# Optimization experiments

Measured on AMD Instinct MI355X. Metric: run time of the kernel, lower is better.

## Reference

```python
import jax, jax.numpy as jnp
import numpy as np
from math import factorial, sqrt

# ---- e3nn-style real Wigner-3j (Clebsch-Gordan) construction ----
L1, L2, LOUT, LMID = 3, 3, 3, 4

def _cg_coef(j1, m1, j2, m2, j3, m3):
    if m1 + m2 != m3:
        return 0.0
    f = factorial
    vmin = max(0, j2 - j3 - m1, j1 - j3 + m2)
    vmax = min(j1 + j2 - j3, j1 - m1, j2 + m2)
    pref = sqrt((2 * j3 + 1) * f(j3 + j1 - j2) * f(j3 - j1 + j2) * f(j1 + j2 - j3) / f(j1 + j2 + j3 + 1))
    pref *= sqrt(f(j3 + m3) * f(j3 - m3) * f(j1 + m1) * f(j1 - m1) * f(j2 + m2) * f(j2 - m2))
    s = 0.0
    for v in range(vmin, vmax + 1):
        s += (-1) ** v / (f(v) * f(j1 + j2 - j3 - v) * f(j1 - m1 - v) * f(j2 + m2 - v)
                          * f(j3 - j2 + m1 + v) * f(j3 - j1 - m2 + v))
    return pref * s

def _su2_cg(l1, l2, l3):
    C = np.zeros((2 * l1 + 1, 2 * l2 + 1, 2 * l3 + 1))
    for m1 in range(-l1, l1 + 1):
        for m2 in range(-l2, l2 + 1):
            m3 = m1 + m2
            if -l3 <= m3 <= l3:
                C[l1 + m1, l2 + m2, l3 + m3] = _cg_coef(l1, m1, l2, m2, l3, m3)
    return C

def _q(l):  # real->complex SH change of basis (e3nn convention)
    q = np.zeros((2 * l + 1, 2 * l + 1), dtype=np.complex128)
    for m in range(-l, 0):
        q[l + m, l + abs(m)] = 1 / np.sqrt(2)
        q[l + m, l - abs(m)] = -1j / np.sqrt(2)
    q[l, l] = 1.0
    for m in range(1, l + 1):
        q[l + m, l + abs(m)] = (-1) ** m / np.sqrt(2)
        q[l + m, l - abs(m)] = 1j * (-1) ** m / np.sqrt(2)
    return (-1j) ** l * q

def _w3j(l1, l2, l3):
    C = _su2_cg(l1, l2, l3).astype(np.complex128)
    C = np.einsum('ij,kl,mn,ikn->jlm', _q(l1), _q(l2), np.conj(_q(l3).T), C)
    C = np.real(C)
    return (C / np.linalg.norm(C)).astype(np.float32)

def _instructions(lmax1, lmax2, lmax_out):
    ins = [(a, b, c)
           for a in range(lmax1 + 1) for b in range(lmax2 + 1) for c in range(lmax_out + 1)
           if abs(a - b) <= c <= a + b and (a + b + c) % 2 == 0]
    cnt = {}
    for _, _, c in ins:
        cnt[c] = cnt.get(c, 0) + 1
    # normalization='component', path_normalization='element' with all mul=1
    pw = np.array([sqrt((2 * c + 1) / cnt[c]) for _, _, c in ins], dtype=np.float32)
    return ins, pw

INS1, PW1 = _instructions(L1, L2, LMID)      # 27 paths
INS21, PW21 = _instructions(L1, LMID, LOUT)  # 27 paths
INS22, PW22 = _instructions(L2, LMID, LOUT)  # 27 paths
W3J = {k: jnp.asarray(_w3j(*k)) for k in set(INS1) | set(INS21) | set(INS22)}

def _tp(x, y, w, ins, pw, lmax_out):
    # FullyConnectedTensorProduct with multiplicity-1 SH irreps.
    # x: [E, (l1+1)^2], y: [E, (l2+1)^2] -> [E, (lmax_out+1)^2]
    out = jnp.zeros((x.shape[0], (lmax_out + 1) ** 2), dtype=x.dtype)
    for i, (a, b, c) in enumerate(ins):
        xa = x[:, a * a:(a + 1) ** 2]
        yb = y[:, b * b:(b + 1) ** 2]
        z = jnp.einsum('ijk,ei,ej->ek', W3J[(a, b, c)], xa, yb)
        out = out.at[:, c * c:(c + 1) ** 2].add((pw[i] * w[i]) * z)
    return out

E, C = 200000, 16
B = (LOUT + 1) ** 2  # 16

def setup_inputs() -> dict:
    k = jax.random.split(jax.random.key(0), 5)
    return {
        'x': jax.random.normal(k[0], (E, B, C), jnp.float32),
        'y': jax.random.normal(k[1], (E, B, C), jnp.float32),
        'w1': jax.random.normal(k[2], (len(INS1),), jnp.float32),
        'w21': jax.random.normal(k[3], (len(INS21),), jnp.float32),
        'w22': jax.random.normal(k[4], (len(INS22),), jnp.float32),
    }

def reference(x, y, w1, w21, w22):
    xm = x.mean(2)  # [E, 16]
    ym = y.mean(2)  # [E, 16]
    mid = _tp(xm, ym, w1, INS1, PW1, LMID)  # [E, 25]
    out = (x + y
           + _tp(xm, mid, w21, INS21, PW21, LOUT)[..., None]
           + _tp(ym, mid, w22, INS22, PW22, LOUT)[..., None])
    return out
```

## Files before the change

### kernel.cpp

```cpp
#include <hip/hip_runtime.h>


struct W3JT { double v[9][9][9]; };

constexpr double dfact(int n) { double r = 1.0; for (int i = 2; i <= n; ++i) r *= (double)i; return r; }

constexpr double csqrt(double x) {
  if (x <= 0.0) return 0.0;
  double g = x > 1.0 ? x : 1.0;
  for (int i = 0; i < 80; ++i) g = 0.5 * (g + x / g);
  return g;
}

constexpr double cg_coef(int j1, int m1, int j2, int m2, int j3, int m3) {
  if (m1 + m2 != m3) return 0.0;
  int vmin = 0;
  if (j2 - j3 - m1 > vmin) vmin = j2 - j3 - m1;
  if (j1 - j3 + m2 > vmin) vmin = j1 - j3 + m2;
  int vmax = j1 + j2 - j3;
  if (j1 - m1 < vmax) vmax = j1 - m1;
  if (j2 + m2 < vmax) vmax = j2 + m2;
  double pref = csqrt((2.0 * j3 + 1.0) * dfact(j3 + j1 - j2) * dfact(j3 - j1 + j2) * dfact(j1 + j2 - j3) / dfact(j1 + j2 + j3 + 1));
  pref *= csqrt(dfact(j3 + m3) * dfact(j3 - m3) * dfact(j1 + m1) * dfact(j1 - m1) * dfact(j2 + m2) * dfact(j2 - m2));
  double s = 0.0;
  for (int v = vmin; v <= vmax; ++v) {
    double t = 1.0 / (dfact(v) * dfact(j1 + j2 - j3 - v) * dfact(j1 - m1 - v) * dfact(j2 + m2 - v) * dfact(j3 - j2 + m1 + v) * dfact(j3 - j1 - m2 + v));
    s += (v & 1) ? -t : t;
  }
  return pref * s;
}

struct QCol { int n; int row[2]; double re[2]; double im[2]; };

constexpr QCol qcol(int l, int col) {
  QCol q{};
  const int lm = l & 3;
  const double pr = (lm == 0) ? 1.0 : (lm == 2) ? -1.0 : 0.0;
  const double pi = (lm == 1) ? -1.0 : (lm == 3) ? 1.0 : 0.0;
  const int mu = col - l;
  const int am = mu < 0 ? -mu : mu;
  const double is2 = 0.70710678118654752440;
  if (mu == 0) {
    q.n = 1; q.row[0] = l;
    q.re[0] = pr; q.im[0] = pi;
  } else {
    const double s = (am & 1) ? -1.0 : 1.0;
    double a0 = 0.0, b0 = 0.0, a1 = 0.0, b1 = 0.0;
    if (mu > 0) { a0 = is2; b0 = 0.0;  a1 = s * is2; b1 = 0.0; }
    else        { a0 = 0.0; b0 = -is2; a1 = 0.0;     b1 = s * is2; }
    q.n = 2;
    q.row[0] = l - am; q.row[1] = l + am;
    q.re[0] = a0 * pr - b0 * pi; q.im[0] = a0 * pi + b0 * pr;
    q.re[1] = a1 * pr - b1 * pi; q.im[1] = a1 * pi + b1 * pr;
  }
  return q;
}

constexpr W3JT make_w3j(int l1, int l2, int l3) {
  W3JT R{};
  double C[9][9][9]{};
  for (int m1 = -l1; m1 <= l1; ++m1)
    for (int m2 = -l2; m2 <= l2; ++m2) {
      int m3 = m1 + m2;
      if (m3 >= -l3 && m3 <= l3)
        C[l1 + m1][l2 + m2][l3 + m3] = cg_coef(l1, m1, l2, m2, l3, m3);
    }
  double nrm = 0.0;
  for (int j = 0; j < 2 * l1 + 1; ++j) {
    QCol q1 = qcol(l1, j);
    for (int l = 0; l < 2 * l2 + 1; ++l) {
      QCol q2 = qcol(l2, l);
      for (int m = 0; m < 2 * l3 + 1; ++m) {
        QCol q3 = qcol(l3, m);
        double re = 0.0;
        for (int a = 0; a < q1.n; ++a)
          for (int b = 0; b < q2.n; ++b)
            for (int c = 0; c < q3.n; ++c) {
              double cv = C[q1.row[a]][q2.row[b]][q3.row[c]];
              if (cv == 0.0) continue;
              double ar = q1.re[a], ai = q1.im[a];
              double br = q2.re[b], bi = q2.im[b];
              double cr = q3.re[c], ci = -q3.im[c];
              double abr = ar * br - ai * bi;
              double abi = ar * bi + ai * br;
              double prr = abr * cr - abi * ci;
              re += prr * cv;
            }
        R.v[j][l][m] = re;
        nrm += re * re;
      }
    }
  }
  double n = csqrt(nrm);
  if (n > 0.0)
    for (int j = 0; j < 2 * l1 + 1; ++j)
      for (int l = 0; l < 2 * l2 + 1; ++l)
        for (int m = 0; m < 2 * l3 + 1; ++m)
          R.v[j][l][m] /= n;
  return R;
}

constexpr int CNT1[5] = {4, 6, 7, 6, 4};
constexpr int CNT2[4] = {4, 7, 8, 8};

#define NZCHK(V) ((V) > 1e-12 || (V) < -1e-12)

#define TP_MID(IDX, A, B, C) do { \
  constexpr W3JT T = make_w3j(A, B, C); \
  constexpr double PW = csqrt((2.0 * (C) + 1.0) / (double)CNT1[(C)]); \
  const float wi = w1p[IDX]; \
  float u[2 * (A) + 1]; \
  _Pragma("unroll") for (int i = 0; i < 2 * (A) + 1; ++i) u[i] = wi * xm[(A) * (A) + i]; \
  _Pragma("unroll") for (int i = 0; i < 2 * (A) + 1; ++i) { \
    _Pragma("unroll") for (int j = 0; j < 2 * (B) + 1; ++j) { \
      const float p_ = u[i] * ym[(B) * (B) + j]; \
      _Pragma("unroll") for (int k = 0; k < 2 * (C) + 1; ++k) { \
        if (NZCHK(T.v[i][j][k])) \
          mid[(C) * (C) + k] = __builtin_fmaf((float)(T.v[i][j][k] * PW), p_, mid[(C) * (C) + k]); \
      } \
    } \
  } \
} while (0)

#define TP_OUT(IDX, A, B, C) do { \
  constexpr W3JT T = make_w3j(A, B, C); \
  constexpr double PW = csqrt((2.0 * (C) + 1.0) / (double)CNT2[(C)]); \
  const float wa = w21p[IDX]; \
  const float wb = w22p[IDX]; \
  float u[2 * (A) + 1]; \
  _Pragma("unroll") for (int i = 0; i < 2 * (A) + 1; ++i) \
    u[i] = wa * xm[(A) * (A) + i] + wb * ym[(A) * (A) + i]; \
  _Pragma("unroll") for (int i = 0; i < 2 * (A) + 1; ++i) { \
    _Pragma("unroll") for (int j = 0; j < 2 * (B) + 1; ++j) { \
      const float p_ = u[i] * mid[(B) * (B) + j]; \
      _Pragma("unroll") for (int k = 0; k < 2 * (C) + 1; ++k) { \
        if (NZCHK(T.v[i][j][k])) \
          tv[(C) * (C) + k] = __builtin_fmaf((float)(T.v[i][j][k] * PW), p_, tv[(C) * (C) + k]); \
      } \
    } \
  } \
} while (0)

__global__ __launch_bounds__(256) void cg2_v6(
    const float4* __restrict__ x4, const float4* __restrict__ y4,
    const float* __restrict__ w1p, const float* __restrict__ w21p,
    const float* __restrict__ w22p, float4* __restrict__ o4, int E)
{
  __shared__ float lmx[64 * 32];
  __shared__ float ltv[64 * 16];

  const int eL = threadIdx.x >> 2;
  const int g  = threadIdx.x & 3;
  const int e  = blockIdx.x * 64 + eL;
  const bool ok = (e < E);
  const int base = e * 64 + g;

  float4 s[16];
  float px[16], py[16];
  if (ok) {
#pragma unroll
    for (int k = 0; k < 16; ++k) {
      const float4 xv = x4[base + 4 * k];
      const float4 yv = y4[base + 4 * k];
      s[k].x = xv.x + yv.x; s[k].y = xv.y + yv.y;
      s[k].z = xv.z + yv.z; s[k].w = xv.w + yv.w;
      px[k] = (xv.x + xv.y) + (xv.z + xv.w);
      py[k] = (yv.x + yv.y) + (yv.z + yv.w);
    }
  } else {
#pragma unroll
    for (int k = 0; k < 16; ++k) { px[k] = 0.f; py[k] = 0.f; }
  }

#pragma unroll
  for (int k = 0; k < 16; ++k) {
    float rx = px[k] + __shfl_xor(px[k], 1);
    rx += __shfl_xor(rx, 2);
    float ry = py[k] + __shfl_xor(py[k], 1);
    ry += __shfl_xor(ry, 2);
    px[k] = rx * (1.0f / 16.0f);
    py[k] = ry * (1.0f / 16.0f);
  }

  if (ok) {
#pragma unroll
    for (int u = 0; u < 4; ++u) {
      const int j = 4 * g + u;
      lmx[eL * 32 + ((j + eL) & 31)]      = px[j];
      lmx[eL * 32 + ((16 + j + eL) & 31)] = py[j];
    }
  }
  __syncthreads();

  if (threadIdx.x < 64) {
    const int q = threadIdx.x;
    const bool ok2 = (blockIdx.x * 64 + q < E);
    float xm[16], ym[16];
#pragma unroll
    for (int j = 0; j < 16; ++j) xm[j] = lmx[q * 32 + ((j + q) & 31)];
#pragma unroll
    for (int j = 0; j < 16; ++j) ym[j] = lmx[q * 32 + ((16 + j + q) & 31)];

    float mid[25];
#pragma unroll
    for (int k = 0; k < 25; ++k) mid[k] = 0.f;

    TP_MID( 0, 0, 0, 0);
    TP_MID( 1, 0, 1, 1);
    TP_MID( 2, 0, 2, 2);
    TP_MID( 3, 0, 3, 3);
    TP_MID( 4, 1, 0, 1);
    TP_MID( 5, 1, 1, 0);
    TP_MID( 6, 1, 1, 2);
    TP_MID( 7, 1, 2, 1);
    TP_MID( 8, 1, 2, 3);
    TP_MID( 9, 1, 3, 2);
    TP_MID(10, 1, 3, 4);
    TP_MID(11, 2, 0, 2);
    TP_MID(12, 2, 1, 1);
    TP_MID(13, 2, 1, 3);
    TP_MID(14, 2, 2, 0);
    TP_MID(15, 2, 2, 2);
    TP_MID(16, 2, 2, 4);
    TP_MID(17, 2, 3, 1);
    TP_MID(18, 2, 3, 3);
    TP_MID(19, 3, 0, 3);
    TP_MID(20, 3, 1, 2);
    TP_MID(21, 3, 1, 4);
    TP_MID(22, 3, 2, 1);
    TP_MID(23, 3, 2, 3);
    TP_MID(24, 3, 3, 0);
    TP_MID(25, 3, 3, 2);
    TP_MID(26, 3, 3, 4);

    float tv[16];
#pragma unroll
    for (int k = 0; k < 16; ++k) tv[k] = 0.f;

    TP_OUT( 0, 0, 0, 0);
    TP_OUT( 1, 0, 1, 1);
    TP_OUT( 2, 0, 2, 2);
    TP_OUT( 3, 0, 3, 3);
    TP_OUT( 4, 1, 0, 1);
    TP_OUT( 5, 1, 1, 0);
    TP_OUT( 6, 1, 1, 2);
    TP_OUT( 7, 1, 2, 1);
    TP_OUT( 8, 1, 2, 3);
    TP_OUT( 9, 1, 3, 2);
    TP_OUT(10, 1, 4, 3);
    TP_OUT(11, 2, 0, 2);
    TP_OUT(12, 2, 1, 1);
    TP_OUT(13, 2, 1, 3);
    TP_OUT(14, 2, 2, 0);
    TP_OUT(15, 2, 2, 2);
    TP_OUT(16, 2, 3, 1);
    TP_OUT(17, 2, 3, 3);
    TP_OUT(18, 2, 4, 2);
    TP_OUT(19, 3, 0, 3);
    TP_OUT(20, 3, 1, 2);
    TP_OUT(21, 3, 2, 1);
    TP_OUT(22, 3, 2, 3);
    TP_OUT(23, 3, 3, 0);
    TP_OUT(24, 3, 3, 2);
    TP_OUT(25, 3, 4, 1);
    TP_OUT(26, 3, 4, 3);

    if (ok2) {
#pragma unroll
      for (int k = 0; k < 16; ++k) ltv[q * 16 + ((k + q) & 15)] = tv[k];
    }
  }
  __syncthreads();

  if (ok) {
#pragma unroll
    for (int k = 0; k < 16; ++k) {
      const float t = ltv[eL * 16 + ((k + eL) & 15)];
      float4 o;
      o.x = s[k].x + t;
      o.y = s[k].y + t;
      o.z = s[k].z + t;
      o.w = s[k].w + t;
      o4[base + 4 * k] = o;
    }
  }
}

extern "C" void kernel_launch(void* const* d_in, const int* in_sizes, int n_in,
                              void* d_out, int out_size, void* d_ws, size_t ws_size,
                              hipStream_t stream) {
  const float4* x4 = (const float4*)d_in[0];
  const float4* y4 = (const float4*)d_in[1];
  const float* w1p = (const float*)d_in[2];
  const float* w21p = (const float*)d_in[3];
  const float* w22p = (const float*)d_in[4];
  float4* o4 = (float4*)d_out;

  const int E = in_sizes[0] / 256;
  const int block = 256;
  const int grid = (E + 63) / 64;

  cg2_v6<<<grid, block, 0, stream>>>(x4, y4, w1p, w21p, w22p, o4, E);
}
```

Before: 127.2 us.

## Split tensor-product work per wavefront and drop block-wide barriers

```diff
diff --git a/kernel.cpp b/kernel.cpp
--- a/kernel.cpp
+++ b/kernel.cpp
@@ -141,19 +141,28 @@
   } \
 } while (0)
 
-__global__ __launch_bounds__(256) void cg2_v6(
+typedef float f32x4 __attribute__((ext_vector_type(4)));
+
+__global__ __launch_bounds__(256) void cg2_v9(
     const float4* __restrict__ x4, const float4* __restrict__ y4,
     const float* __restrict__ w1p, const float* __restrict__ w21p,
     const float* __restrict__ w22p, float4* __restrict__ o4, int E)
 {
-  __shared__ float lmx[64 * 32];
-  __shared__ float ltv[64 * 16];
-
-  const int eL = threadIdx.x >> 2;
-  const int g  = threadIdx.x & 3;
-  const int e  = blockIdx.x * 64 + eL;
+  __shared__ __align__(16) float spx[4][16 * 68];
+  __shared__ __align__(16) float spy[4][16 * 68];
+  __shared__ float stv[4][16 * 17];
+
+  const int wid = threadIdx.x >> 6;
+  const int l   = threadIdx.x & 63;
+  const int e16 = l >> 2;
+  const int g   = l & 3;
+  const int e   = blockIdx.x * 64 + wid * 16 + e16;
   const bool ok = (e < E);
   const int base = e * 64 + g;
+
+  float* const px_w = &spx[wid][0];
+  float* const py_w = &spy[wid][0];
+  float* const tv_w = &stv[wid][0];
 
   float4 s[16];
   float px[16], py[16];
@@ -172,34 +181,40 @@
     for (int k = 0; k < 16; ++k) { px[k] = 0.f; py[k] = 0.f; }
   }
 
-#pragma unroll
-  for (int k = 0; k < 16; ++k) {
-    float rx = px[k] + __shfl_xor(px[k], 1);
-    rx += __shfl_xor(rx, 2);
-    float ry = py[k] + __shfl_xor(py[k], 1);
-    ry += __shfl_xor(ry, 2);
-    px[k] = rx * (1.0f / 16.0f);
-    py[k] = ry * (1.0f / 16.0f);
-  }
-
-  if (ok) {
-#pragma unroll
-    for (int u = 0; u < 4; ++u) {
-      const int j = 4 * g + u;
-      lmx[eL * 32 + ((j + eL) & 31)]      = px[j];
-      lmx[eL * 32 + ((16 + j + eL) & 31)] = py[j];
-    }
-  }
-  __syncthreads();
-
-  if (threadIdx.x < 64) {
-    const int q = threadIdx.x;
-    const bool ok2 = (blockIdx.x * 64 + q < E);
+  {
+    const int o = e16 * 68 + g * 16;
+#pragma unroll
+    for (int j = 0; j < 4; ++j) {
+      f32x4 vx = { px[4 * j], px[4 * j + 1], px[4 * j + 2], px[4 * j + 3] };
+      f32x4 vy = { py[4 * j], py[4 * j + 1], py[4 * j + 2], py[4 * j + 3] };
+      *(f32x4*)&px_w[o + 4 * j] = vx;
+      *(f32x4*)&py_w[o + 4 * j] = vy;
+    }
+  }
+
+  if (l < 16) {
+    const int q = l;
     float xm[16], ym[16];
 #pragma unroll
-    for (int j = 0; j < 16; ++j) xm[j] = lmx[q * 32 + ((j + q) & 31)];
-#pragma unroll
-    for (int j = 0; j < 16; ++j) ym[j] = lmx[q * 32 + ((16 + j + q) & 31)];
+    for (int j = 0; j < 4; ++j) {
+      const int o = q * 68 + 4 * j;
+      const f32x4 a0 = *(const f32x4*)&px_w[o];
+      const f32x4 a1 = *(const f32x4*)&px_w[o + 16];
+      const f32x4 a2 = *(const f32x4*)&px_w[o + 32];
+      const f32x4 a3 = *(const f32x4*)&px_w[o + 48];
+      xm[4 * j + 0] = ((a0.x + a1.x) + (a2.x + a3.x)) * (1.0f / 16.0f);
+      xm[4 * j + 1] = ((a0.y + a1.y) + (a2.y + a3.y)) * (1.0f / 16.0f);
+      xm[4 * j + 2] = ((a0.z + a1.z) + (a2.z + a3.z)) * (1.0f / 16.0f);
+      xm[4 * j + 3] = ((a0.w + a1.w) + (a2.w + a3.w)) * (1.0f / 16.0f);
+      const f32x4 b0 = *(const f32x4*)&py_w[o];
+      const f32x4 b1 = *(const f32x4*)&py_w[o + 16];
+      const f32x4 b2 = *(const f32x4*)&py_w[o + 32];
+      const f32x4 b3 = *(const f32x4*)&py_w[o + 48];
+      ym[4 * j + 0] = ((b0.x + b1.x) + (b2.x + b3.x)) * (1.0f / 16.0f);
+      ym[4 * j + 1] = ((b0.y + b1.y) + (b2.y + b3.y)) * (1.0f / 16.0f);
+      ym[4 * j + 2] = ((b0.z + b1.z) + (b2.z + b3.z)) * (1.0f / 16.0f);
+      ym[4 * j + 3] = ((b0.w + b1.w) + (b2.w + b3.w)) * (1.0f / 16.0f);
+    }
 
     float mid[25];
 #pragma unroll
@@ -265,17 +280,14 @@
     TP_OUT(25, 3, 4, 1);
     TP_OUT(26, 3, 4, 3);
 
-    if (ok2) {
-#pragma unroll
-      for (int k = 0; k < 16; ++k) ltv[q * 16 + ((k + q) & 15)] = tv[k];
-    }
-  }
-  __syncthreads();
+#pragma unroll
+    for (int k = 0; k < 16; ++k) tv_w[q * 17 + k] = tv[k];
+  }
 
   if (ok) {
 #pragma unroll
     for (int k = 0; k < 16; ++k) {
-      const float t = ltv[eL * 16 + ((k + eL) & 15)];
+      const float t = tv_w[e16 * 17 + k];
       float4 o;
       o.x = s[k].x + t;
       o.y = s[k].y + t;
@@ -300,5 +312,5 @@
   const int block = 256;
   const int grid = (E + 63) / 64;
 
-  cg2_v6<<<grid, block, 0, stream>>>(x4, y4, w1p, w21p, w22p, o4, E);
-}
+  cg2_v9<<<grid, block, 0, stream>>>(x4, y4, w1p, w21p, w22p, o4, E);
+}
```

Result: slower. 185.4 us (+45.8%).
